# Kernel optimization log

Hardware: AMD Instinct MI355X
Metric: run time of the kernel (lower is better)

Reference implementation:

```python
import jax, jax.numpy as jnp
import numpy as np

B, MAX_T, S, H, NB, NA = 64, 511, 1024, 4096, 8, 4


def setup_inputs() -> dict:
    key = jax.random.key(0)
    k1, k2, k3, k4, k5 = jax.random.split(key, 5)
    s_i_batch = jax.random.normal(k1, (B, MAX_T + 1, S), dtype=jnp.float32)
    actions_batch = jax.random.randint(k2, (B, MAX_T), 0, NA, dtype=jnp.int32)
    lengths = jax.random.randint(k3, (B,), 0, MAX_T, dtype=jnp.int32)
    W1 = jax.random.normal(k4, (S, H), dtype=jnp.float32) * (1.0 / np.sqrt(S))
    b1 = jnp.zeros((H,), dtype=jnp.float32)
    W2 = jax.random.normal(k5, (H, NB * NA), dtype=jnp.float32) * (1.0 / np.sqrt(H))
    b2 = jnp.zeros((NB * NA,), dtype=jnp.float32)
    return {"s_i_batch": s_i_batch, "actions_batch": actions_batch,
            "lengths": lengths, "W1": W1, "b1": b1, "W2": W2, "b2": b2}


def reference(s_i_batch, actions_batch, lengths, W1, b1, W2, b2):
    Bc, Tp1, _ = s_i_batch.shape
    maxT = Tp1 - 1
    # control_net: MLP -> per-(option, action) log-probs
    h = jax.nn.relu(jnp.einsum('bts,sh->bth', s_i_batch, W1) + b1)
    logits = (jnp.einsum('bth,ha->bta', h, W2) + b2).reshape(Bc, Tp1, NB, NA)
    action_logps = jax.nn.log_softmax(logits, axis=-1)  # (B, T+1, b, 4)
    # option 0, timesteps 0..max_T-1
    lp0 = action_logps[:, :maxT, 0, :]                  # (B, max_T, 4)
    gathered = jnp.take_along_axis(lp0, actions_batch[..., None].astype(jnp.int32), axis=-1)[..., 0]
    mask = (jnp.arange(maxT)[None, :] < lengths[:, None]).astype(lp0.dtype)  # (B, max_T)
    total_logp = jnp.sum(gathered * mask)
    return -total_logp
```

## Files before the change

### kernel.cpp

```cpp
#include <hip/hip_runtime.h>
#include <hip/hip_bf16.h>
#include <math.h>

#define B_    64
#define MAXT  511
#define TP1   512
#define S_    1024
#define H_    4096
#define M_TOTAL (B_*TP1)
#define NITER (S_/32)

typedef __attribute__((ext_vector_type(8))) short  short8;
typedef __attribute__((ext_vector_type(4))) float  float4v;

#define ZBUF_BYTES ((size_t)M_TOTAL*4*sizeof(float))
#define SBF_OFF    0x81000
#define SBF_BYTES  ((size_t)M_TOTAL*S_*2)
#define W1T_OFF    (SBF_OFF + SBF_BYTES)

static __device__ __forceinline__ unsigned short f2bf(float f) {
    unsigned int u = __float_as_uint(f);
    u = u + 0x7fffu + ((u >> 16) & 1u);
    return (unsigned short)(u >> 16);
}

__global__ __launch_bounds__(256) void prep_kernel(const float* __restrict__ s,
                                                   const float* __restrict__ W1,
                                                   const int*   __restrict__ lengths,
                                                   unsigned short* __restrict__ Sb,
                                                   unsigned short* __restrict__ W1T) {
    int bid = blockIdx.x;
    if (bid < 16384) {
        int row = 2 * bid + (threadIdx.x >> 7);
        int b = row >> 9, t = row & 511;
        if (t >= lengths[b]) return;
        size_t idx = (size_t)row * S_ + (threadIdx.x & 127) * 8;
        float4v f0 = __builtin_nontemporal_load((const float4v*)(s + idx));
        float4v f1 = __builtin_nontemporal_load((const float4v*)(s + idx + 4));
        short8 o;
        o[0] = (short)f2bf(f0[0]); o[1] = (short)f2bf(f0[1]);
        o[2] = (short)f2bf(f0[2]); o[3] = (short)f2bf(f0[3]);
        o[4] = (short)f2bf(f1[0]); o[5] = (short)f2bf(f1[1]);
        o[6] = (short)f2bf(f1[2]); o[7] = (short)f2bf(f1[3]);
        *(short8*)(Sb + idx) = o;
    } else {
        __shared__ float tile[32][33];
        int tb = bid - 16384;
        int h0 = (tb & 127) * 32;
        int k0 = (tb >> 7) * 32;
        int tx = threadIdx.x & 31, ty = threadIdx.x >> 5;
        for (int r = ty; r < 32; r += 8)
            tile[r][tx] = __builtin_nontemporal_load(&W1[(size_t)(k0 + r) * H_ + h0 + tx]);
        __syncthreads();
        for (int r = ty; r < 32; r += 8)
            W1T[(size_t)(h0 + r) * S_ + k0 + tx] = f2bf(tile[tx][r]);
    }
}

__global__ __launch_bounds__(256, 3) void gemm_fused_kernel(
        const unsigned short* __restrict__ Sb,
        const unsigned short* __restrict__ W1T,
        const float* __restrict__ b1,
        const float* __restrict__ W2,
        const int*   __restrict__ lengths,
        float*       __restrict__ zbuf)
{
    int id   = blockIdx.x;
    int xcd  = id & 7;
    int slot = id >> 3;
    int ntile = xcd * 4 + (slot & 3);
    int mtile = slot >> 2;

    int b  = mtile >> 2;
    int t0 = (mtile & 3) * 128;
    if (lengths[b] <= t0) return;

    int m0 = mtile * 128;
    int n0 = ntile * 128;

    __shared__ unsigned short smemA[2 * 128 * 32];
    __shared__ unsigned short smemB[2 * 128 * 32];

    int tid  = threadIdx.x;
    int wid  = tid >> 6;
    int lane = tid & 63;
    int lane15 = lane & 15;
    int quad   = lane >> 4;
    int wave_m = (wid >> 1) * 64;
    int wave_n = (wid & 1) * 64;

    int cA0 = tid, cA1 = tid + 256;
    int mA0 = cA0 >> 2, cp0 = cA0 & 3, q0 = cp0 ^ ((mA0 >> 1) & 3);
    int mA1 = cA1 >> 2, cp1 = cA1 & 3, q1 = cp1 ^ ((mA1 >> 1) & 3);

    const char* gA0 = (const char*)Sb  + (size_t)(m0 + mA0) * (S_*2) + q0 * 16;
    const char* gA1 = (const char*)Sb  + (size_t)(m0 + mA1) * (S_*2) + q1 * 16;
    const char* gB0 = (const char*)W1T + (size_t)(n0 + mA0) * (S_*2) + q0 * 16;
    const char* gB1 = (const char*)W1T + (size_t)(n0 + mA1) * (S_*2) + q1 * 16;
    char* lwA0 = (char*)smemA + cA0 * 16;
    char* lwA1 = (char*)smemA + cA1 * 16;
    char* lwB0 = (char*)smemB + cA0 * 16;
    char* lwB1 = (char*)smemB + cA1 * 16;

    int aOff[4], bOff[4];
#pragma unroll
    for (int s = 0; s < 4; s++) {
        int ml = wave_m + s * 16 + lane15;
        aOff[s] = ml * 32 + (quad ^ ((ml >> 1) & 3)) * 8;
        int nl = wave_n + s * 16 + lane15;
        bOff[s] = nl * 32 + (quad ^ ((nl >> 1) & 3)) * 8;
    }

    float4v acc[4][4] = {};
    short8 sA0[3], sA1[3], sB0[3], sB1[3];

#pragma unroll
    for (int p = 0; p < 3; p++) {
        sA0[p] = *(const short8*)(gA0 + p * 64);
        sA1[p] = *(const short8*)(gA1 + p * 64);
        sB0[p] = *(const short8*)(gB0 + p * 64);
        sB1[p] = *(const short8*)(gB1 + p * 64);
    }
    *(short8*)lwA0 = sA0[0]; *(short8*)lwA1 = sA1[0];
    *(short8*)lwB0 = sB0[0]; *(short8*)lwB1 = sB1[0];

#pragma unroll
    for (int j = 0; j < NITER; j++) {
        __syncthreads();
        if (j + 3 < NITER) {
            sA0[j % 3] = *(const short8*)(gA0 + (j + 3) * 64);
            sA1[j % 3] = *(const short8*)(gA1 + (j + 3) * 64);
            sB0[j % 3] = *(const short8*)(gB0 + (j + 3) * 64);
            sB1[j % 3] = *(const short8*)(gB1 + (j + 3) * 64);
        }
        if (j + 1 < NITER) {
            int nb = ((j + 1) & 1) * 8192;
            *(short8*)(lwA0 + nb) = sA0[(j + 1) % 3];
            *(short8*)(lwA1 + nb) = sA1[(j + 1) % 3];
            *(short8*)(lwB0 + nb) = sB0[(j + 1) % 3];
            *(short8*)(lwB1 + nb) = sB1[(j + 1) % 3];
        }
        const unsigned short* aP = smemA + (j & 1) * 4096;
        const unsigned short* bP = smemB + (j & 1) * 4096;
        short8 af[4], bf[4];
#pragma unroll
        for (int s = 0; s < 4; s++) {
            af[s] = *(const short8*)(aP + aOff[s]);
            bf[s] = *(const short8*)(bP + bOff[s]);
        }
#pragma unroll
        for (int i = 0; i < 4; i++)
#pragma unroll
            for (int jj = 0; jj < 4; jj++)
                acc[i][jj] = __builtin_amdgcn_mfma_f32_16x16x32_bf16(af[i], bf[jj], acc[i][jj], 0, 0, 0);
    }

    float4v w2r[4];
    float   b1v[4];
#pragma unroll
    for (int ns = 0; ns < 4; ns++) {
        int n_g = n0 + wave_n + ns * 16 + lane15;
        w2r[ns] = *(const float4v*)(W2 + (size_t)n_g * 32);
        b1v[ns] = b1[n_g];
    }
#pragma unroll
    for (int ms = 0; ms < 4; ms++) {
        float p[4][4];
#pragma unroll
        for (int r = 0; r < 4; r++)
#pragma unroll
            for (int c = 0; c < 4; c++) p[r][c] = 0.f;
#pragma unroll
        for (int ns = 0; ns < 4; ns++) {
            float4v av = acc[ms][ns];
#pragma unroll
            for (int r = 0; r < 4; r++) {
                float h = av[r] + b1v[ns];
                h = h > 0.f ? h : 0.f;
                p[r][0] += h * w2r[ns][0];
                p[r][1] += h * w2r[ns][1];
                p[r][2] += h * w2r[ns][2];
                p[r][3] += h * w2r[ns][3];
            }
        }
#pragma unroll
        for (int off = 1; off < 16; off <<= 1)
#pragma unroll
            for (int r = 0; r < 4; r++)
#pragma unroll
                for (int c = 0; c < 4; c++)
                    p[r][c] += __shfl_xor(p[r][c], off);
        if (lane15 < 4) {
            int c = lane15;
#pragma unroll
            for (int r = 0; r < 4; r++) {
                int mg = m0 + wave_m + ms * 16 + quad * 4 + r;
                atomicAdd(&zbuf[(size_t)mg * 4 + c], p[r][c]);
            }
        }
    }
}

__global__ __launch_bounds__(128) void reduce_logp_kernel(
        const float* __restrict__ zbuf,
        const int*   __restrict__ actions,
        const int*   __restrict__ lengths,
        const float* __restrict__ b2,
        float*       __restrict__ out)
{
    int b = blockIdx.x;
    int t = blockIdx.y * 128 + threadIdx.x;
    int len = lengths[b];
    float local = 0.f;
    if (t < MAXT && t < len) {
        int row = b * TP1 + t;
        float4v z = *(const float4v*)(zbuf + (size_t)row * 4);
        float z0 = z[0] + b2[0], z1 = z[1] + b2[1], z2 = z[2] + b2[2], z3 = z[3] + b2[3];
        float mx = fmaxf(fmaxf(z0, z1), fmaxf(z2, z3));
        float se = expf(z0 - mx) + expf(z1 - mx) + expf(z2 - mx) + expf(z3 - mx);
        int a = actions[b * MAXT + t];
        float za = (a == 0) ? z0 : (a == 1) ? z1 : (a == 2) ? z2 : z3;
        local = (za - mx) - logf(se);
    }
#pragma unroll
    for (int off = 32; off > 0; off >>= 1) local += __shfl_xor(local, off);
    __shared__ float wsum[2];
    if ((threadIdx.x & 63) == 0) wsum[threadIdx.x >> 6] = local;
    __syncthreads();
    if (threadIdx.x == 0) atomicAdd(out, -(wsum[0] + wsum[1]));
}

extern "C" void kernel_launch(void* const* d_in, const int* in_sizes, int n_in,
                              void* d_out, int out_size, void* d_ws, size_t ws_size,
                              hipStream_t stream) {
    const float* s       = (const float*)d_in[0];
    const int*   actions = (const int*)  d_in[1];
    const int*   lengths = (const int*)  d_in[2];
    const float* W1      = (const float*)d_in[3];
    const float* b1      = (const float*)d_in[4];
    const float* W2      = (const float*)d_in[5];
    const float* b2      = (const float*)d_in[6];

    char* ws = (char*)d_ws;
    float*          zbuf = (float*)ws;
    unsigned short* Sb   = (unsigned short*)(ws + SBF_OFF);
    unsigned short* W1T  = (unsigned short*)(ws + W1T_OFF);

    hipMemsetAsync(ws, 0, ZBUF_BYTES, stream);
    hipMemsetAsync(d_out, 0, sizeof(float), stream);

    prep_kernel<<<dim3(16384 + 4096), 256, 0, stream>>>(s, W1, lengths, Sb, W1T);
    gemm_fused_kernel<<<dim3(8192), 256, 0, stream>>>(Sb, W1T, b1, W2, lengths, zbuf);
    reduce_logp_kernel<<<dim3(B_, 4), 128, 0, stream>>>(zbuf, actions, lengths, b2, (float*)d_out);
}
```

Before: 474.0 us.

## Rewrite fused GEMM with 256x256 tiles and direct global-to-LDS loads

Replaces the 128x128 tile GEMM, which staged data through registers, with a 256x256 tile, 8-wave kernel. Operands are loaded with global_load_lds straight into a swizzled double-buffered LDS, and MFMA phases are interleaved with fragment loads using barriers, sched_barrier and setprio. This aims to raise arithmetic intensity per tile and overlap memory with compute. In exchange the length-based early exit becomes coarser (256 rows), the grid is smaller, and register pressure and occupancy change.

```diff
diff --git a/kernel.cpp b/kernel.cpp
--- a/kernel.cpp
+++ b/kernel.cpp
@@ -1,5 +1,4 @@
 #include <hip/hip_runtime.h>
-#include <hip/hip_bf16.h>
 #include <math.h>
 
 #define B_    64
@@ -8,7 +7,7 @@
 #define S_    1024
 #define H_    4096
 #define M_TOTAL (B_*TP1)
-#define NITER (S_/32)
+#define NT    (S_/64)
 
 typedef __attribute__((ext_vector_type(8))) short  short8;
 typedef __attribute__((ext_vector_type(4))) float  float4v;
@@ -57,7 +56,14 @@
     }
 }
 
-__global__ __launch_bounds__(256, 3) void gemm_fused_kernel(
+typedef __attribute__((address_space(1))) unsigned int gu32;
+typedef __attribute__((address_space(3))) unsigned int lu32;
+static __device__ __forceinline__ void gload16(const void* g, void* l) {
+    __builtin_amdgcn_global_load_lds((gu32*)g, (lu32*)l, 16, 0, 0);
+}
+static __device__ __forceinline__ short8 ld8(const char* p) { return *(const short8*)p; }
+
+__global__ __launch_bounds__(512, 2) void gemm_fused_kernel(
         const unsigned short* __restrict__ Sb,
         const unsigned short* __restrict__ W1T,
         const float* __restrict__ b1,
@@ -65,140 +71,171 @@
         const int*   __restrict__ lengths,
         float*       __restrict__ zbuf)
 {
-    int id   = blockIdx.x;
-    int xcd  = id & 7;
-    int slot = id >> 3;
-    int ntile = xcd * 4 + (slot & 3);
-    int mtile = slot >> 2;
-
-    int b  = mtile >> 2;
-    int t0 = (mtile & 3) * 128;
-    if (lengths[b] <= t0) return;
-
-    int m0 = mtile * 128;
-    int n0 = ntile * 128;
-
-    __shared__ unsigned short smemA[2 * 128 * 32];
-    __shared__ unsigned short smemB[2 * 128 * 32];
-
-    int tid  = threadIdx.x;
-    int wid  = tid >> 6;
-    int lane = tid & 63;
-    int lane15 = lane & 15;
-    int quad   = lane >> 4;
-    int wave_m = (wid >> 1) * 64;
-    int wave_n = (wid & 1) * 64;
-
-    int cA0 = tid, cA1 = tid + 256;
-    int mA0 = cA0 >> 2, cp0 = cA0 & 3, q0 = cp0 ^ ((mA0 >> 1) & 3);
-    int mA1 = cA1 >> 2, cp1 = cA1 & 3, q1 = cp1 ^ ((mA1 >> 1) & 3);
-
-    const char* gA0 = (const char*)Sb  + (size_t)(m0 + mA0) * (S_*2) + q0 * 16;
-    const char* gA1 = (const char*)Sb  + (size_t)(m0 + mA1) * (S_*2) + q1 * 16;
-    const char* gB0 = (const char*)W1T + (size_t)(n0 + mA0) * (S_*2) + q0 * 16;
-    const char* gB1 = (const char*)W1T + (size_t)(n0 + mA1) * (S_*2) + q1 * 16;
-    char* lwA0 = (char*)smemA + cA0 * 16;
-    char* lwA1 = (char*)smemA + cA1 * 16;
-    char* lwB0 = (char*)smemB + cA0 * 16;
-    char* lwB1 = (char*)smemB + cA1 * 16;
-
-    int aOff[4], bOff[4];
-#pragma unroll
-    for (int s = 0; s < 4; s++) {
-        int ml = wave_m + s * 16 + lane15;
-        aOff[s] = ml * 32 + (quad ^ ((ml >> 1) & 3)) * 8;
-        int nl = wave_n + s * 16 + lane15;
-        bOff[s] = nl * 32 + (quad ^ ((nl >> 1) & 3)) * 8;
-    }
-
-    float4v acc[4][4] = {};
-    short8 sA0[3], sA1[3], sB0[3], sB1[3];
-
-#pragma unroll
-    for (int p = 0; p < 3; p++) {
-        sA0[p] = *(const short8*)(gA0 + p * 64);
-        sA1[p] = *(const short8*)(gA1 + p * 64);
-        sB0[p] = *(const short8*)(gB0 + p * 64);
-        sB1[p] = *(const short8*)(gB1 + p * 64);
-    }
-    *(short8*)lwA0 = sA0[0]; *(short8*)lwA1 = sA1[0];
-    *(short8*)lwB0 = sB0[0]; *(short8*)lwB1 = sB1[0];
-
-#pragma unroll
-    for (int j = 0; j < NITER; j++) {
-        __syncthreads();
-        if (j + 3 < NITER) {
-            sA0[j % 3] = *(const short8*)(gA0 + (j + 3) * 64);
-            sA1[j % 3] = *(const short8*)(gA1 + (j + 3) * 64);
-            sB0[j % 3] = *(const short8*)(gB0 + (j + 3) * 64);
-            sB1[j % 3] = *(const short8*)(gB1 + (j + 3) * 64);
-        }
-        if (j + 1 < NITER) {
-            int nb = ((j + 1) & 1) * 8192;
-            *(short8*)(lwA0 + nb) = sA0[(j + 1) % 3];
-            *(short8*)(lwA1 + nb) = sA1[(j + 1) % 3];
-            *(short8*)(lwB0 + nb) = sB0[(j + 1) % 3];
-            *(short8*)(lwB1 + nb) = sB1[(j + 1) % 3];
-        }
-        const unsigned short* aP = smemA + (j & 1) * 4096;
-        const unsigned short* bP = smemB + (j & 1) * 4096;
-        short8 af[4], bf[4];
-#pragma unroll
-        for (int s = 0; s < 4; s++) {
-            af[s] = *(const short8*)(aP + aOff[s]);
-            bf[s] = *(const short8*)(bP + bOff[s]);
-        }
-#pragma unroll
-        for (int i = 0; i < 4; i++)
-#pragma unroll
-            for (int jj = 0; jj < 4; jj++)
-                acc[i][jj] = __builtin_amdgcn_mfma_f32_16x16x32_bf16(af[i], bf[jj], acc[i][jj], 0, 0, 0);
+    int id  = blockIdx.x;
+    int xcd = id & 7;
+    int sl  = id >> 3;
+    int ntile = xcd * 2 + (sl >> 7);
+    int mtile = sl & 127;
+    int bi = mtile >> 1;
+    if (lengths[bi] <= (mtile & 1) * 256) return;
+    int m0 = mtile * 256;
+    int n0 = ntile * 256;
+
+    __shared__ unsigned short lds[2][2][16384];
+    char* L = (char*)lds;
+
+    int tid = threadIdx.x;
+    int wid = tid >> 6, lane = tid & 63;
+    int lane15 = lane & 15, quad = lane >> 4;
+    int wave_m = (wid >> 2) * 128;
+    int wave_n = (wid & 3) * 64;
+
+    int smask = (lane15 & 7) << 4;
+    int c0 = (quad * 16) ^ smask;
+    int c1 = (64 + quad * 16) ^ smask;
+    int aRow = (wave_m + lane15) * 128;
+    int bRow = (wave_n + lane15) * 128;
+
+    int srow = tid >> 3;
+    int scol = ((tid & 7) * 16) ^ ((srow & 7) << 4);
+    const char* gAs = (const char*)Sb  + (size_t)(m0 + srow) * 2048 + scol;
+    const char* gBs = (const char*)W1T + (size_t)(n0 + srow) * 2048 + scol;
+    char* dA = L + wid * 1024;
+    char* dB = L + 32768 + wid * 1024;
+
+#define STAGE_A(bb,h,tt) do { \
+    const char* g_ = gAs + (h)*262144 + (tt)*128; \
+    char* d_ = dA + (bb)*65536 + (h)*16384; \
+    gload16(g_, d_); gload16(g_ + 131072, d_ + 8192); } while(0)
+#define STAGE_B(bb,h,tt) do { \
+    const char* g_ = gBs + (h)*262144 + (tt)*128; \
+    char* d_ = dB + (bb)*65536 + (h)*16384; \
+    gload16(g_, d_); gload16(g_ + 131072, d_ + 8192); } while(0)
+
+    float4v acc[8][4] = {};
+    short8 af[4][2], bfr[4][2];
+
+    STAGE_B(0,0,0); STAGE_B(0,1,0); STAGE_A(0,0,0); STAGE_A(0,1,0);
+    STAGE_B(1,0,1); STAGE_B(1,1,1);
+    asm volatile("s_waitcnt vmcnt(4)" ::: "memory");
+    __builtin_amdgcn_sched_barrier(0);
+    __builtin_amdgcn_s_barrier();
+
+#define MFMA16(MH, NF0) \
+    _Pragma("unroll") for (int mf = 0; mf < 4; ++mf) \
+    _Pragma("unroll") for (int nf = 0; nf < 2; ++nf) \
+    _Pragma("unroll") for (int kk = 0; kk < 2; ++kk) \
+        acc[(MH)*4+mf][(NF0)+nf] = __builtin_amdgcn_mfma_f32_16x16x32_bf16( \
+            af[mf][kk], bfr[(NF0)+nf][kk], acc[(MH)*4+mf][(NF0)+nf], 0, 0, 0)
+
+#define PH_BEGIN() \
+    __builtin_amdgcn_s_barrier(); \
+    asm volatile("s_waitcnt lgkmcnt(0)" ::: "memory"); \
+    __builtin_amdgcn_sched_barrier(0); \
+    __builtin_amdgcn_s_setprio(1)
+#define PH_END() \
+    __builtin_amdgcn_s_setprio(0); \
+    __builtin_amdgcn_sched_barrier(0); \
+    __builtin_amdgcn_s_barrier()
+
+#pragma unroll 2
+    for (int t = 0; t < NT; ++t) {
+        int bb = t & 1;
+        const char* A  = L + bb * 65536;
+        const char* Bm = A + 32768;
+#pragma unroll
+        for (int mf = 0; mf < 4; ++mf) {
+            af[mf][0] = ld8(A + aRow + mf*2048 + c0);
+            af[mf][1] = ld8(A + aRow + mf*2048 + c1);
+        }
+#pragma unroll
+        for (int nf = 0; nf < 2; ++nf) {
+            bfr[nf][0] = ld8(Bm + bRow + nf*2048 + c0);
+            bfr[nf][1] = ld8(Bm + bRow + nf*2048 + c1);
+        }
+        if (t + 1 < NT) STAGE_A(bb^1, 0, t+1);
+        PH_BEGIN();
+        MFMA16(0, 0);
+        PH_END();
+#pragma unroll
+        for (int nf = 2; nf < 4; ++nf) {
+            bfr[nf][0] = ld8(Bm + bRow + nf*2048 + c0);
+            bfr[nf][1] = ld8(Bm + bRow + nf*2048 + c1);
+        }
+        if (t + 1 < NT) STAGE_A(bb^1, 1, t+1);
+        PH_BEGIN();
+        MFMA16(0, 2);
+        PH_END();
+#pragma unroll
+        for (int mf = 0; mf < 4; ++mf) {
+            af[mf][0] = ld8(A + aRow + 8192 + mf*2048 + c0);
+            af[mf][1] = ld8(A + aRow + 8192 + mf*2048 + c1);
+        }
+        if (t + 2 < NT) STAGE_B(bb, 0, t+2);
+        PH_BEGIN();
+        MFMA16(1, 2);
+        PH_END();
+        if (t + 2 < NT) STAGE_B(bb, 1, t+2);
+        __builtin_amdgcn_s_barrier();
+        __builtin_amdgcn_sched_barrier(0);
+        __builtin_amdgcn_s_setprio(1);
+        MFMA16(1, 0);
+        __builtin_amdgcn_s_setprio(0);
+        __builtin_amdgcn_sched_barrier(0);
+        if (t < NT - 2)       { asm volatile("s_waitcnt vmcnt(4)" ::: "memory"); __builtin_amdgcn_sched_barrier(0); }
+        else if (t == NT - 2) { asm volatile("s_waitcnt vmcnt(0)" ::: "memory"); __builtin_amdgcn_sched_barrier(0); }
+        __builtin_amdgcn_s_barrier();
     }
 
     float4v w2r[4];
     float   b1v[4];
 #pragma unroll
-    for (int ns = 0; ns < 4; ns++) {
-        int n_g = n0 + wave_n + ns * 16 + lane15;
-        w2r[ns] = *(const float4v*)(W2 + (size_t)n_g * 32);
-        b1v[ns] = b1[n_g];
-    }
-#pragma unroll
-    for (int ms = 0; ms < 4; ms++) {
+    for (int nf = 0; nf < 4; ++nf) {
+        int n_g = n0 + wave_n + nf * 16 + lane15;
+        w2r[nf] = *(const float4v*)(W2 + (size_t)n_g * 32);
+        b1v[nf] = b1[n_g];
+    }
+#pragma unroll
+    for (int ms = 0; ms < 8; ++ms) {
         float p[4][4];
 #pragma unroll
-        for (int r = 0; r < 4; r++)
-#pragma unroll
-            for (int c = 0; c < 4; c++) p[r][c] = 0.f;
-#pragma unroll
-        for (int ns = 0; ns < 4; ns++) {
-            float4v av = acc[ms][ns];
-#pragma unroll
-            for (int r = 0; r < 4; r++) {
-                float h = av[r] + b1v[ns];
+        for (int r = 0; r < 4; ++r)
+#pragma unroll
+            for (int c = 0; c < 4; ++c) p[r][c] = 0.f;
+#pragma unroll
+        for (int nf = 0; nf < 4; ++nf) {
+            float4v av = acc[ms][nf];
+#pragma unroll
+            for (int r = 0; r < 4; ++r) {
+                float h = av[r] + b1v[nf];
                 h = h > 0.f ? h : 0.f;
-                p[r][0] += h * w2r[ns][0];
-                p[r][1] += h * w2r[ns][1];
-                p[r][2] += h * w2r[ns][2];
-                p[r][3] += h * w2r[ns][3];
+                p[r][0] += h * w2r[nf][0];
+                p[r][1] += h * w2r[nf][1];
+                p[r][2] += h * w2r[nf][2];
+                p[r][3] += h * w2r[nf][3];
             }
         }
 #pragma unroll
         for (int off = 1; off < 16; off <<= 1)
 #pragma unroll
-            for (int r = 0; r < 4; r++)
-#pragma unroll
-                for (int c = 0; c < 4; c++)
+            for (int r = 0; r < 4; ++r)
+#pragma unroll
+                for (int c = 0; c < 4; ++c)
                     p[r][c] += __shfl_xor(p[r][c], off);
         if (lane15 < 4) {
             int c = lane15;
 #pragma unroll
-            for (int r = 0; r < 4; r++) {
+            for (int r = 0; r < 4; ++r) {
                 int mg = m0 + wave_m + ms * 16 + quad * 4 + r;
                 atomicAdd(&zbuf[(size_t)mg * 4 + c], p[r][c]);
             }
         }
     }
+#undef STAGE_A
+#undef STAGE_B
+#undef MFMA16
+#undef PH_BEGIN
+#undef PH_END
 }
 
 __global__ __launch_bounds__(128) void reduce_logp_kernel(
@@ -250,6 +287,6 @@
     hipMemsetAsync(d_out, 0, sizeof(float), stream);
 
     prep_kernel<<<dim3(16384 + 4096), 256, 0, stream>>>(s, W1, lengths, Sb, W1T);
-    gemm_fused_kernel<<<dim3(8192), 256, 0, stream>>>(Sb, W1T, b1, W2, lengths, zbuf);
+    gemm_fused_kernel<<<dim3(2048), 512, 0, stream>>>(Sb, W1T, b1, W2, lengths, zbuf);
     reduce_logp_kernel<<<dim3(B_, 4), 128, 0, stream>>>(zbuf, actions, lengths, b2, (float*)d_out);
 }
```

New measurement: 573.6 us. 1.21x slower.

## Load GEMM tiles directly into LDS with global_load_lds and raise occupancy

Applied to the files above, without the earlier changes.

Replaces the register-staged triple-buffered prefetch (global load to VGPRs, then LDS store) with direct global-to-LDS 16-byte loads into a double buffer, issuing the next stage before computing the current one. This removes the VGPR staging registers and the LDS write instructions. Launch bounds go from 3 to 4 blocks per SM, since register pressure drops. The cost is a shallower prefetch (one stage ahead instead of three) and reliance on the barrier at the end of each iteration to cover the async LDS-load completion.

```diff
diff --git a/kernel.cpp b/kernel.cpp
--- a/kernel.cpp
+++ b/kernel.cpp
@@ -1,5 +1,4 @@
 #include <hip/hip_runtime.h>
-#include <hip/hip_bf16.h>
 #include <math.h>
 
 #define B_    64
@@ -57,7 +56,13 @@
     }
 }
 
-__global__ __launch_bounds__(256, 3) void gemm_fused_kernel(
+typedef __attribute__((address_space(1))) unsigned int gu32;
+typedef __attribute__((address_space(3))) unsigned int lu32;
+static __device__ __forceinline__ void gload16(const void* g, void* l) {
+    __builtin_amdgcn_global_load_lds((gu32*)g, (lu32*)l, 16, 0, 0);
+}
+
+__global__ __launch_bounds__(256, 4) void gemm_fused_kernel(
         const unsigned short* __restrict__ Sb,
         const unsigned short* __restrict__ W1T,
         const float* __restrict__ b1,
@@ -90,8 +95,8 @@
     int wave_n = (wid & 1) * 64;
 
     int cA0 = tid, cA1 = tid + 256;
-    int mA0 = cA0 >> 2, cp0 = cA0 & 3, q0 = cp0 ^ ((mA0 >> 1) & 3);
-    int mA1 = cA1 >> 2, cp1 = cA1 & 3, q1 = cp1 ^ ((mA1 >> 1) & 3);
+    int mA0 = cA0 >> 2, q0 = (cA0 & 3) ^ ((mA0 >> 1) & 3);
+    int mA1 = cA1 >> 2, q1 = (cA1 & 3) ^ ((mA1 >> 1) & 3);
 
     const char* gA0 = (const char*)Sb  + (size_t)(m0 + mA0) * (S_*2) + q0 * 16;
     const char* gA1 = (const char*)Sb  + (size_t)(m0 + mA1) * (S_*2) + q1 * 16;
@@ -111,35 +116,21 @@
         bOff[s] = nl * 32 + (quad ^ ((nl >> 1) & 3)) * 8;
     }
 
+#define STAGE(bufsel, jj) do { \
+    int off_ = (jj) * 64; int lb_ = (bufsel) * 8192; \
+    gload16(gA0 + off_, lwA0 + lb_); \
+    gload16(gA1 + off_, lwA1 + lb_); \
+    gload16(gB0 + off_, lwB0 + lb_); \
+    gload16(gB1 + off_, lwB1 + lb_); \
+} while (0)
+
     float4v acc[4][4] = {};
-    short8 sA0[3], sA1[3], sB0[3], sB1[3];
-
-#pragma unroll
-    for (int p = 0; p < 3; p++) {
-        sA0[p] = *(const short8*)(gA0 + p * 64);
-        sA1[p] = *(const short8*)(gA1 + p * 64);
-        sB0[p] = *(const short8*)(gB0 + p * 64);
-        sB1[p] = *(const short8*)(gB1 + p * 64);
-    }
-    *(short8*)lwA0 = sA0[0]; *(short8*)lwA1 = sA1[0];
-    *(short8*)lwB0 = sB0[0]; *(short8*)lwB1 = sB1[0];
-
-#pragma unroll
+
+    STAGE(0, 0);
+    __syncthreads();
+
     for (int j = 0; j < NITER; j++) {
-        __syncthreads();
-        if (j + 3 < NITER) {
-            sA0[j % 3] = *(const short8*)(gA0 + (j + 3) * 64);
-            sA1[j % 3] = *(const short8*)(gA1 + (j + 3) * 64);
-            sB0[j % 3] = *(const short8*)(gB0 + (j + 3) * 64);
-            sB1[j % 3] = *(const short8*)(gB1 + (j + 3) * 64);
-        }
-        if (j + 1 < NITER) {
-            int nb = ((j + 1) & 1) * 8192;
-            *(short8*)(lwA0 + nb) = sA0[(j + 1) % 3];
-            *(short8*)(lwA1 + nb) = sA1[(j + 1) % 3];
-            *(short8*)(lwB0 + nb) = sB0[(j + 1) % 3];
-            *(short8*)(lwB1 + nb) = sB1[(j + 1) % 3];
-        }
+        if (j + 1 < NITER) STAGE((j + 1) & 1, j + 1);
         const unsigned short* aP = smemA + (j & 1) * 4096;
         const unsigned short* bP = smemB + (j & 1) * 4096;
         short8 af[4], bf[4];
@@ -153,7 +144,9 @@
 #pragma unroll
             for (int jj = 0; jj < 4; jj++)
                 acc[i][jj] = __builtin_amdgcn_mfma_f32_16x16x32_bf16(af[i], bf[jj], acc[i][jj], 0, 0, 0);
-    }
+        __syncthreads();
+    }
+#undef STAGE
 
     float4v w2r[4];
     float   b1v[4];
```

Result: slower. 486.3 us (+2.6%).

## Compact valid rows across batches to eliminate padded GEMM tiles

Applied to the files above, without the earlier changes.

Adds a small prefix-sum kernel over the sequence lengths. The prep kernel now writes only valid timesteps into a densely packed bf16 activation buffer, so the GEMM covers a contiguous range of valid rows instead of padded 128-row tiles per batch element. This is meant to remove the wasted MFMA work on partially filled tiles at each sequence tail. In exchange it adds an extra tiny kernel launch and an index indirection. The last tile may compute on stale rows beyond the valid total, but those rows are never read.

```diff
diff --git a/kernel.cpp b/kernel.cpp
--- a/kernel.cpp
+++ b/kernel.cpp
@@ -1,5 +1,4 @@
 #include <hip/hip_runtime.h>
-#include <hip/hip_bf16.h>
 #include <math.h>
 
 #define B_    64
@@ -14,6 +13,7 @@
 typedef __attribute__((ext_vector_type(4))) float  float4v;
 
 #define ZBUF_BYTES ((size_t)M_TOTAL*4*sizeof(float))
+#define OFFS_OFF   0x80000
 #define SBF_OFF    0x81000
 #define SBF_BYTES  ((size_t)M_TOTAL*S_*2)
 #define W1T_OFF    (SBF_OFF + SBF_BYTES)
@@ -24,9 +24,24 @@
     return (unsigned short)(u >> 16);
 }
 
+__global__ __launch_bounds__(64) void offsets_kernel(const int* __restrict__ lengths,
+                                                     int* __restrict__ offs) {
+    int lane = threadIdx.x;
+    int v = lengths[lane];
+    int x = v;
+#pragma unroll
+    for (int d = 1; d < 64; d <<= 1) {
+        int y = __shfl_up(x, d);
+        if (lane >= d) x += y;
+    }
+    offs[lane] = x - v;
+    if (lane == 63) offs[64] = x;
+}
+
 __global__ __launch_bounds__(256) void prep_kernel(const float* __restrict__ s,
                                                    const float* __restrict__ W1,
                                                    const int*   __restrict__ lengths,
+                                                   const int*   __restrict__ offs,
                                                    unsigned short* __restrict__ Sb,
                                                    unsigned short* __restrict__ W1T) {
     int bid = blockIdx.x;
@@ -34,15 +49,17 @@
         int row = 2 * bid + (threadIdx.x >> 7);
         int b = row >> 9, t = row & 511;
         if (t >= lengths[b]) return;
-        size_t idx = (size_t)row * S_ + (threadIdx.x & 127) * 8;
-        float4v f0 = __builtin_nontemporal_load((const float4v*)(s + idx));
-        float4v f1 = __builtin_nontemporal_load((const float4v*)(s + idx + 4));
+        int crow = offs[b] + t;
+        size_t src = (size_t)row  * S_ + (threadIdx.x & 127) * 8;
+        size_t dst = (size_t)crow * S_ + (threadIdx.x & 127) * 8;
+        float4v f0 = __builtin_nontemporal_load((const float4v*)(s + src));
+        float4v f1 = __builtin_nontemporal_load((const float4v*)(s + src + 4));
         short8 o;
         o[0] = (short)f2bf(f0[0]); o[1] = (short)f2bf(f0[1]);
         o[2] = (short)f2bf(f0[2]); o[3] = (short)f2bf(f0[3]);
         o[4] = (short)f2bf(f1[0]); o[5] = (short)f2bf(f1[1]);
         o[6] = (short)f2bf(f1[2]); o[7] = (short)f2bf(f1[3]);
-        *(short8*)(Sb + idx) = o;
+        *(short8*)(Sb + dst) = o;
     } else {
         __shared__ float tile[32][33];
         int tb = bid - 16384;
@@ -62,7 +79,7 @@
         const unsigned short* __restrict__ W1T,
         const float* __restrict__ b1,
         const float* __restrict__ W2,
-        const int*   __restrict__ lengths,
+        const int*   __restrict__ offs,
         float*       __restrict__ zbuf)
 {
     int id   = blockIdx.x;
@@ -71,11 +88,9 @@
     int ntile = xcd * 4 + (slot & 3);
     int mtile = slot >> 2;
 
-    int b  = mtile >> 2;
-    int t0 = (mtile & 3) * 128;
-    if (lengths[b] <= t0) return;
-
     int m0 = mtile * 128;
+    if (m0 >= offs[64]) return;
+
     int n0 = ntile * 128;
 
     __shared__ unsigned short smemA[2 * 128 * 32];
@@ -205,6 +220,7 @@
         const float* __restrict__ zbuf,
         const int*   __restrict__ actions,
         const int*   __restrict__ lengths,
+        const int*   __restrict__ offs,
         const float* __restrict__ b2,
         float*       __restrict__ out)
 {
@@ -213,7 +229,7 @@
     int len = lengths[b];
     float local = 0.f;
     if (t < MAXT && t < len) {
-        int row = b * TP1 + t;
+        int row = offs[b] + t;
         float4v z = *(const float4v*)(zbuf + (size_t)row * 4);
         float z0 = z[0] + b2[0], z1 = z[1] + b2[1], z2 = z[2] + b2[2], z3 = z[3] + b2[3];
         float mx = fmaxf(fmaxf(z0, z1), fmaxf(z2, z3));
@@ -243,13 +259,15 @@
 
     char* ws = (char*)d_ws;
     float*          zbuf = (float*)ws;
+    int*            offs = (int*)(ws + OFFS_OFF);
     unsigned short* Sb   = (unsigned short*)(ws + SBF_OFF);
     unsigned short* W1T  = (unsigned short*)(ws + W1T_OFF);
 
     hipMemsetAsync(ws, 0, ZBUF_BYTES, stream);
     hipMemsetAsync(d_out, 0, sizeof(float), stream);
 
-    prep_kernel<<<dim3(16384 + 4096), 256, 0, stream>>>(s, W1, lengths, Sb, W1T);
-    gemm_fused_kernel<<<dim3(8192), 256, 0, stream>>>(Sb, W1T, b1, W2, lengths, zbuf);
-    reduce_logp_kernel<<<dim3(B_, 4), 128, 0, stream>>>(zbuf, actions, lengths, b2, (float*)d_out);
-}
+    offsets_kernel<<<dim3(1), 64, 0, stream>>>(lengths, offs);
+    prep_kernel<<<dim3(16384 + 4096), 256, 0, stream>>>(s, W1, lengths, offs, Sb, W1T);
+    gemm_fused_kernel<<<dim3(8192), 256, 0, stream>>>(Sb, W1T, b1, W2, offs, zbuf);
+    reduce_logp_kernel<<<dim3(B_, 4), 128, 0, stream>>>(zbuf, actions, lengths, offs, b2, (float*)d_out);
+}
```

Result: faster. 426.0 us (-10.1%).
